# Kernel tuning notes

Measured on AMD Instinct MI355X. Metric: run time of the kernel, lower is better.

## Reference

```python
import jax, jax.numpy as jnp
import numpy as np

N_USERS = 100000
N_MOVIES = 50000
N_EDGES = 1000000
IN_CH, HID, OUT = 64, 128, 64


def setup_inputs() -> dict:
    key = jax.random.key(0)
    ks = jax.random.split(key, 8)
    N = N_USERS + N_MOVIES
    return {
        "edge_index": jax.random.randint(ks[0], (2, N_EDGES), 0, N, dtype=jnp.int64)
        if jax.config.jax_enable_x64 else jax.random.randint(ks[0], (2, N_EDGES), 0, N, dtype=jnp.int32),
        "user_emb": jax.random.normal(ks[1], (N_USERS, IN_CH), jnp.float32) * 0.05,
        "movie_emb": jax.random.normal(ks[2], (N_MOVIES, IN_CH), jnp.float32) * 0.05,
        "W1l": jax.random.normal(ks[3], (HID, IN_CH), jnp.float32) * 0.05,
        "b1": jnp.zeros((HID,), jnp.float32),
        "W1r": jax.random.normal(ks[4], (HID, IN_CH), jnp.float32) * 0.05,
        "W2l": jax.random.normal(ks[5], (OUT, HID), jnp.float32) * 0.05,
        "b2": jnp.zeros((OUT,), jnp.float32),
        "W2r": jax.random.normal(ks[6], (OUT, HID), jnp.float32) * 0.05,
    }


def _sage_conv(x, src, dst, Wl, bl, Wr, num_nodes):
    # mean-aggregate neighbor (source) features at destination nodes
    msg_sum = jax.ops.segment_sum(x[src], dst, num_segments=num_nodes)  # [N, d_in]
    deg = jax.ops.segment_sum(jnp.ones(src.shape, x.dtype), dst, num_segments=num_nodes)
    agg = msg_sum / jnp.maximum(deg, 1.0)[:, None]
    # out = lin_l(agg) + lin_r(x); lin_l carries the bias (PyG SAGEConv default)
    return agg @ Wl.T + bl + x @ Wr.T


def reference(edge_index, user_emb, movie_emb, W1l, b1, W1r, W2l, b2, W2r):
    N = user_emb.shape[0] + movie_emb.shape[0]
    src, dst = edge_index[0], edge_index[1]
    x = jnp.concatenate([user_emb, movie_emb], axis=0)  # [N, in_ch]
    x = jax.nn.relu(_sage_conv(x, src, dst, W1l, b1, W1r, N))  # dropout = identity (eval)
    x = _sage_conv(x, src, dst, W2l, b2, W2r, N)
    return x[:N_USERS], x[N_USERS:]
```

## Files before the change

### kernel.cpp

```cpp
#include <hip/hip_runtime.h>

constexpr int N_USERS  = 100000;
constexpr int N_MOVIES = 50000;
constexpr int N_NODES  = N_USERS + N_MOVIES;
constexpr int N_EDGES  = 1000000;

typedef __attribute__((ext_vector_type(8))) short bf16x8;
typedef __attribute__((ext_vector_type(8))) unsigned short usx8;
typedef __attribute__((ext_vector_type(4))) float f32x4;

__device__ inline unsigned short bf16_rne(float x) {
    unsigned u = __float_as_uint(x);
    unsigned r = (u + 0x7FFF + ((u >> 16) & 1)) >> 16;
    return (unsigned short)r;
}
__device__ inline float bf16_to_f(short v) {
    return __uint_as_float(((unsigned)(unsigned short)v) << 16);
}

__global__ __launch_bounds__(256) void csr_ord(const int* __restrict__ ei,
                                               int* __restrict__ cnt,
                                               int* __restrict__ ord) {
    int t  = blockIdx.x * 256 + threadIdx.x;
    int e0 = t * 4;
    if (e0 + 3 < N_EDGES) {
        int4 d = *(const int4*)&ei[N_EDGES + e0];
        int4 o;
        o.x = atomicAdd(&cnt[d.x], 1);
        o.y = atomicAdd(&cnt[d.y], 1);
        o.z = atomicAdd(&cnt[d.z], 1);
        o.w = atomicAdd(&cnt[d.w], 1);
        *(int4*)&ord[e0] = o;
    } else {
        for (int e = e0; e < N_EDGES; ++e)
            ord[e] = atomicAdd(&cnt[ei[N_EDGES + e]], 1);
    }
}

__global__ __launch_bounds__(256) void csr_scatter(const int* __restrict__ ei,
                                                   const int* __restrict__ row_ptr,
                                                   const int* __restrict__ ord,
                                                   int* __restrict__ srclist) {
    int t  = blockIdx.x * 256 + threadIdx.x;
    int e0 = t * 4;
    if (e0 + 3 < N_EDGES) {
        int4 s = *(const int4*)&ei[e0];
        int4 d = *(const int4*)&ei[N_EDGES + e0];
        int4 o = *(const int4*)&ord[e0];
        srclist[row_ptr[d.x] + o.x] = s.x;
        srclist[row_ptr[d.y] + o.y] = s.y;
        srclist[row_ptr[d.z] + o.z] = s.z;
        srclist[row_ptr[d.w] + o.w] = s.w;
    } else {
        for (int e = e0; e < N_EDGES; ++e)
            srclist[row_ptr[ei[N_EDGES + e]] + ord[e]] = ei[e];
    }
}

__global__ __launch_bounds__(256) void scan1(const int* __restrict__ cnt,
                                             int* __restrict__ part,
                                             int* __restrict__ bsum) {
    __shared__ int sh[256];
    int t = threadIdx.x, b = blockIdx.x;
    int base = b * 1024 + t * 4;
    int v[4]; int s = 0;
#pragma unroll
    for (int j = 0; j < 4; ++j) {
        int i = base + j;
        v[j] = (i < N_NODES) ? cnt[i] : 0;
        s += v[j];
    }
    sh[t] = s; __syncthreads();
    for (int off = 1; off < 256; off <<= 1) {
        int x = (t >= off) ? sh[t - off] : 0;
        __syncthreads();
        sh[t] += x;
        __syncthreads();
    }
    int run = sh[t] - s;
#pragma unroll
    for (int j = 0; j < 4; ++j) {
        int i = base + j;
        if (i < N_NODES) part[i] = run;
        run += v[j];
    }
    if (t == 255) bsum[b] = sh[255];
}

__global__ __launch_bounds__(256) void scan2(int* __restrict__ bsum, int nb) {
    __shared__ int sh[256];
    int t = threadIdx.x;
    int v = (t < nb) ? bsum[t] : 0;
    sh[t] = v; __syncthreads();
    for (int off = 1; off < 256; off <<= 1) {
        int x = (t >= off) ? sh[t - off] : 0;
        __syncthreads();
        sh[t] += x;
        __syncthreads();
    }
    if (t < nb) bsum[t] = sh[t] - v;
}

__global__ __launch_bounds__(256) void scan3(int* __restrict__ row_ptr,
                                             const int* __restrict__ bsum) {
    int t = threadIdx.x, b = blockIdx.x;
    int base = b * 1024 + t * 4;
    int add = bsum[b];
#pragma unroll
    for (int j = 0; j < 4; ++j) {
        int i = base + j;
        if (i < N_NODES) row_ptr[i] += add;
    }
    if (b == 0 && t == 0) row_ptr[N_NODES] = N_EDGES;
}

__global__ __launch_bounds__(256) void prepack_w(const float* __restrict__ W1l,
                                                 const float* __restrict__ W1r,
                                                 const float* __restrict__ W2l,
                                                 const float* __restrict__ W2r,
                                                 unsigned short* __restrict__ wb) {
    int i = blockIdx.x * 256 + threadIdx.x;
    if (i >= 2 * 128 * 128) return;
    int layer = i >> 14;
    int r     = i & 16383;
    int kc    = r >> 12;
    int oc    = (r >> 9) & 7;
    int lane  = (r >> 3) & 63;
    int j     = r & 7;
    int k = kc * 32 + (lane >> 4) * 8 + j;
    int o = oc * 16 + (lane & 15);
    float v;
    if (layer == 0) v = (k < 64) ? W1l[o * 64 + k] : W1r[o * 64 + (k - 64)];
    else            v = (o < 64) ? W2l[o * 128 + k] : W2r[(o - 64) * 128 + k];
    wb[i] = bf16_rne(v);
}

__global__ __launch_bounds__(256) void pack_x(const float* __restrict__ ue,
                                              const float* __restrict__ me,
                                              unsigned short* __restrict__ xb) {
    int i = blockIdx.x * 256 + threadIdx.x;
    if (i >= N_NODES * 8) return;
    int n = i >> 3, c = (i & 7) * 8;
    const float* src = (n < N_USERS) ? &ue[(size_t)n * 64 + c]
                                     : &me[(size_t)(n - N_USERS) * 64 + c];
    float4 v0 = *(const float4*)src;
    float4 v1 = *(const float4*)(src + 4);
    usx8 r;
    r[0] = bf16_rne(v0.x); r[1] = bf16_rne(v0.y);
    r[2] = bf16_rne(v0.z); r[3] = bf16_rne(v0.w);
    r[4] = bf16_rne(v1.x); r[5] = bf16_rne(v1.y);
    r[6] = bf16_rne(v1.z); r[7] = bf16_rne(v1.w);
    *(usx8*)&xb[(size_t)n * 64 + c] = r;
}

__global__ __launch_bounds__(256) void gather1(const int* __restrict__ row_ptr,
                                               const int* __restrict__ srclist,
                                               const unsigned short* __restrict__ xb,
                                               unsigned short* __restrict__ aggb) {
    int gid = blockIdx.x * 256 + threadIdx.x;
    int n = gid >> 3, l = gid & 7;
    if (n >= N_NODES) return;
    int s0 = row_ptr[n], s1 = row_ptr[n + 1];
    float acc[8] = {};
    for (int i = s0; i < s1; ++i) {
        int a = srclist[i];
        bf16x8 v = *(const bf16x8*)&xb[(size_t)a * 64 + l * 8];
#pragma unroll
        for (int j = 0; j < 8; ++j) acc[j] += bf16_to_f(v[j]);
    }
    float inv = 1.0f / fmaxf((float)(s1 - s0), 1.0f);
    usx8 r;
#pragma unroll
    for (int j = 0; j < 8; ++j) r[j] = bf16_rne(acc[j] * inv);
    *(usx8*)&aggb[(size_t)n * 64 + l * 8] = r;
}

__global__ __launch_bounds__(256) void gather2_final(const int* __restrict__ row_ptr,
                                                     const int* __restrict__ srclist,
                                                     const unsigned short* __restrict__ zb,
                                                     const float* __restrict__ wf,
                                                     const float* __restrict__ b2,
                                                     float* __restrict__ out) {
    int gid = blockIdx.x * 256 + threadIdx.x;
    int n = gid >> 3, l = gid & 7;
    if (n >= N_NODES) return;
    int s0 = row_ptr[n], s1 = row_ptr[n + 1];
    float acc[8] = {};
    for (int i = s0; i < s1; ++i) {
        int a = srclist[i];
        bf16x8 v = *(const bf16x8*)&zb[(size_t)a * 64 + l * 8];
#pragma unroll
        for (int j = 0; j < 8; ++j) acc[j] += bf16_to_f(v[j]);
    }
    float inv = 1.0f / fmaxf((float)(s1 - s0), 1.0f);
    float4 w0 = *(const float4*)&wf[(size_t)n * 64 + l * 8];
    float4 w1 = *(const float4*)&wf[(size_t)n * 64 + l * 8 + 4];
    float4 c0 = *(const float4*)&b2[l * 8];
    float4 c1 = *(const float4*)&b2[l * 8 + 4];
    float4 r0, r1;
    r0.x = acc[0] * inv + w0.x + c0.x;
    r0.y = acc[1] * inv + w0.y + c0.y;
    r0.z = acc[2] * inv + w0.z + c0.z;
    r0.w = acc[3] * inv + w0.w + c0.w;
    r1.x = acc[4] * inv + w1.x + c1.x;
    r1.y = acc[5] * inv + w1.y + c1.y;
    r1.z = acc[6] * inv + w1.z + c1.z;
    r1.w = acc[7] * inv + w1.w + c1.w;
    *(float4*)&out[(size_t)n * 64 + l * 8]     = r0;
    *(float4*)&out[(size_t)n * 64 + l * 8 + 4] = r1;
}

template <bool LAYER1>
__global__ __launch_bounds__(256) void gemm_bf16(const unsigned short* Ab,
                                                 const unsigned short* __restrict__ xb,
                                                 const unsigned short* __restrict__ wb,
                                                 const float* __restrict__ bias,
                                                 unsigned short* outb,
                                                 float* outf) {
    const int tid  = threadIdx.x;
    const int w    = tid >> 6;
    const int lane = tid & 63;
    const int n0   = blockIdx.x * 128 + w * 32;
    const int lr   = lane & 15;
    const int lg   = lane >> 4;

    f32x4 acc[2][8] = {};
    const int wbase = LAYER1 ? 0 : 2048;

    for (int kc = 0; kc < 4; ++kc) {
        const int k0 = kc * 32 + lg * 8;
        bf16x8 a[2];
#pragma unroll
        for (int f = 0; f < 2; ++f) {
            int node = n0 + f * 16 + lr;
            bf16x8 z = {};
            a[f] = z;
            if (node < N_NODES) {
                const unsigned short* ap;
                if (LAYER1)
                    ap = (k0 < 64) ? &Ab[(size_t)node * 64 + k0]
                                   : &xb[(size_t)node * 64 + (k0 - 64)];
                else
                    ap = &Ab[(size_t)node * 128 + k0];
                a[f] = *(const bf16x8*)ap;
            }
        }
#pragma unroll
        for (int oc = 0; oc < 8; ++oc) {
            size_t widx = ((size_t)(wbase + (kc * 8 + oc) * 64 + lane)) * 8;
            bf16x8 wfrag = *(const bf16x8*)&wb[widx];
#pragma unroll
            for (int f = 0; f < 2; ++f)
                acc[f][oc] = __builtin_amdgcn_mfma_f32_16x16x32_bf16(a[f], wfrag, acc[f][oc], 0, 0, 0);
        }
    }

#pragma unroll
    for (int f = 0; f < 2; ++f) {
#pragma unroll
        for (int oc = 0; oc < 8; ++oc) {
            int col = oc * 16 + lr;
            float b = LAYER1 ? bias[col] : 0.f;
#pragma unroll
            for (int i = 0; i < 4; ++i) {
                int row = n0 + f * 16 + lg * 4 + i;
                if (row < N_NODES) {
                    float v = acc[f][oc][i] + b;
                    if (LAYER1) {
                        outb[(size_t)row * 128 + col] = bf16_rne(fmaxf(v, 0.f));
                    } else {
                        if (oc < 4) outb[(size_t)row * 64 + col] = bf16_rne(v);
                        else        outf[(size_t)row * 64 + (col - 64)] = v;
                    }
                }
            }
        }
    }
}

extern "C" void kernel_launch(void* const* d_in, const int* in_sizes, int n_in,
                              void* d_out, int out_size, void* d_ws, size_t ws_size,
                              hipStream_t stream) {
    const int*   ei  = (const int*)d_in[0];
    const float* ue  = (const float*)d_in[1];
    const float* me  = (const float*)d_in[2];
    const float* W1l = (const float*)d_in[3];
    const float* b1  = (const float*)d_in[4];
    const float* W1r = (const float*)d_in[5];
    const float* W2l = (const float*)d_in[6];
    const float* b2  = (const float*)d_in[7];
    const float* W2r = (const float*)d_in[8];
    float* out = (float*)d_out;

    char* p = (char*)d_ws;
    int* row_ptr = (int*)p;                   p += (((N_NODES + 1) * 4) + 255) / 256 * 256;
    int* srclist = (int*)p;                   p += (size_t)N_EDGES * 4;
    int* ord     = (int*)p;                   p += (size_t)N_EDGES * 4;
    unsigned short* wb = (unsigned short*)p;  p += 2 * 128 * 128 * 2;
    unsigned short* xb = (unsigned short*)p;  p += (size_t)N_NODES * 64 * 2;
    unsigned short* h1b = (unsigned short*)p; p += (size_t)N_NODES * 128 * 2;
    unsigned short* zb  = (unsigned short*)p; p += (size_t)N_NODES * 64 * 2;
    float* wf = (float*)h1b;
    int* cnt  = (int*)h1b;
    int* bsum = cnt + N_NODES;
    unsigned short* aggb = (unsigned short*)out;

    const int NB  = (N_NODES + 1023) / 1024;
    const int EB4 = (N_EDGES / 4 + 255) / 256;

    hipMemsetAsync(cnt, 0, N_NODES * sizeof(int), stream);
    csr_ord<<<EB4, 256, 0, stream>>>(ei, cnt, ord);
    scan1<<<NB, 256, 0, stream>>>(cnt, row_ptr, bsum);
    scan2<<<1, 256, 0, stream>>>(bsum, NB);
    scan3<<<NB, 256, 0, stream>>>(row_ptr, bsum);
    csr_scatter<<<EB4, 256, 0, stream>>>(ei, row_ptr, ord, srclist);
    prepack_w<<<(2 * 128 * 128 + 255) / 256, 256, 0, stream>>>(W1l, W1r, W2l, W2r, wb);
    pack_x<<<(N_NODES * 8 + 255) / 256, 256, 0, stream>>>(ue, me, xb);

    int gblocks = (N_NODES * 8 + 255) / 256;
    int mblocks = (N_NODES + 127) / 128;

    gather1<<<gblocks, 256, 0, stream>>>(row_ptr, srclist, xb, aggb);
    gemm_bf16<true><<<mblocks, 256, 0, stream>>>(aggb, xb, wb, b1, h1b, nullptr);
    gemm_bf16<false><<<mblocks, 256, 0, stream>>>(h1b, nullptr, wb, nullptr, zb, wf);
    gather2_final<<<gblocks, 256, 0, stream>>>(row_ptr, srclist, zb, wf, b2, out);
}
```

Measured before the change: 206.8 us.

## Fuse both GEMM layers via LDS and merge prep and scan kernels

The two layer GEMMs now run in one kernel: the ReLU'd hidden tile is kept in shared memory and fed straight into the second GEMM, so the 128-wide hidden activation never goes to global memory. Edge counting, weight prepacking and embedding conversion are merged into one launch, and the second and third scan passes are combined, with each block redoing the small block-sum scan itself. The root-term output of layer 2 is now stored as bf16 instead of fp32, which halves that traffic but adds rounding error to the final output. Fewer launches and less global memory traffic are the aim, at the cost of more LDS per block, which may lower occupancy.

```diff
diff --git a/kernel.cpp b/kernel.cpp
--- a/kernel.cpp
+++ b/kernel.cpp
@@ -18,23 +18,127 @@
     return __uint_as_float(((unsigned)(unsigned short)v) << 16);
 }
 
-__global__ __launch_bounds__(256) void csr_ord(const int* __restrict__ ei,
-                                               int* __restrict__ cnt,
-                                               int* __restrict__ ord) {
-    int t  = blockIdx.x * 256 + threadIdx.x;
-    int e0 = t * 4;
-    if (e0 + 3 < N_EDGES) {
-        int4 d = *(const int4*)&ei[N_EDGES + e0];
-        int4 o;
-        o.x = atomicAdd(&cnt[d.x], 1);
-        o.y = atomicAdd(&cnt[d.y], 1);
-        o.z = atomicAdd(&cnt[d.z], 1);
-        o.w = atomicAdd(&cnt[d.w], 1);
-        *(int4*)&ord[e0] = o;
-    } else {
-        for (int e = e0; e < N_EDGES; ++e)
-            ord[e] = atomicAdd(&cnt[ei[N_EDGES + e]], 1);
-    }
+constexpr int ORD_BLKS = (N_EDGES / 8 + 255) / 256;
+constexpr int PW_BLKS  = (2 * 128 * 128) / 256;
+constexpr int PX_BLKS  = (N_NODES * 8 + 255) / 256;
+
+__global__ __launch_bounds__(256) void prep_fused(const int* __restrict__ ei,
+                                                  int* __restrict__ cnt,
+                                                  int* __restrict__ ord,
+                                                  const float* __restrict__ W1l,
+                                                  const float* __restrict__ W1r,
+                                                  const float* __restrict__ W2l,
+                                                  const float* __restrict__ W2r,
+                                                  unsigned short* __restrict__ wb,
+                                                  const float* __restrict__ ue,
+                                                  const float* __restrict__ me,
+                                                  unsigned short* __restrict__ xb) {
+    const int ob = blockIdx.x;
+    if (ob < ORD_BLKS) {
+        int t  = ob * 256 + threadIdx.x;
+        int e0 = t * 8;
+        if (e0 + 7 < N_EDGES) {
+            int4 d0 = *(const int4*)&ei[N_EDGES + e0];
+            int4 d1 = *(const int4*)&ei[N_EDGES + e0 + 4];
+            int4 o0, o1;
+            o0.x = atomicAdd(&cnt[d0.x], 1);
+            o0.y = atomicAdd(&cnt[d0.y], 1);
+            o0.z = atomicAdd(&cnt[d0.z], 1);
+            o0.w = atomicAdd(&cnt[d0.w], 1);
+            o1.x = atomicAdd(&cnt[d1.x], 1);
+            o1.y = atomicAdd(&cnt[d1.y], 1);
+            o1.z = atomicAdd(&cnt[d1.z], 1);
+            o1.w = atomicAdd(&cnt[d1.w], 1);
+            *(int4*)&ord[e0]     = o0;
+            *(int4*)&ord[e0 + 4] = o1;
+        } else {
+            for (int e = e0; e < N_EDGES; ++e)
+                ord[e] = atomicAdd(&cnt[ei[N_EDGES + e]], 1);
+        }
+        return;
+    }
+    if (ob < ORD_BLKS + PW_BLKS) {
+        int i = (ob - ORD_BLKS) * 256 + threadIdx.x;
+        int layer = i >> 14;
+        int r     = i & 16383;
+        int kc    = r >> 12;
+        int oc    = (r >> 9) & 7;
+        int lane  = (r >> 3) & 63;
+        int j     = r & 7;
+        int k = kc * 32 + (lane >> 4) * 8 + j;
+        int o = oc * 16 + (lane & 15);
+        float v;
+        if (layer == 0) v = (k < 64) ? W1l[o * 64 + k] : W1r[o * 64 + (k - 64)];
+        else            v = (o < 64) ? W2l[o * 128 + k] : W2r[(o - 64) * 128 + k];
+        wb[i] = bf16_rne(v);
+        return;
+    }
+    int i = (ob - ORD_BLKS - PW_BLKS) * 256 + threadIdx.x;
+    if (i >= N_NODES * 8) return;
+    int n = i >> 3, c = (i & 7) * 8;
+    const float* src = (n < N_USERS) ? &ue[(size_t)n * 64 + c]
+                                     : &me[(size_t)(n - N_USERS) * 64 + c];
+    float4 v0 = *(const float4*)src;
+    float4 v1 = *(const float4*)(src + 4);
+    usx8 r;
+    r[0] = bf16_rne(v0.x); r[1] = bf16_rne(v0.y);
+    r[2] = bf16_rne(v0.z); r[3] = bf16_rne(v0.w);
+    r[4] = bf16_rne(v1.x); r[5] = bf16_rne(v1.y);
+    r[6] = bf16_rne(v1.z); r[7] = bf16_rne(v1.w);
+    *(usx8*)&xb[(size_t)n * 64 + c] = r;
+}
+
+__global__ __launch_bounds__(256) void scan1(const int* __restrict__ cnt,
+                                             int* __restrict__ part,
+                                             int* __restrict__ bsum) {
+    __shared__ int sh[256];
+    int t = threadIdx.x, b = blockIdx.x;
+    int base = b * 1024 + t * 4;
+    int v[4]; int s = 0;
+#pragma unroll
+    for (int j = 0; j < 4; ++j) {
+        int i = base + j;
+        v[j] = (i < N_NODES) ? cnt[i] : 0;
+        s += v[j];
+    }
+    sh[t] = s; __syncthreads();
+    for (int off = 1; off < 256; off <<= 1) {
+        int x = (t >= off) ? sh[t - off] : 0;
+        __syncthreads();
+        sh[t] += x;
+        __syncthreads();
+    }
+    int run = sh[t] - s;
+#pragma unroll
+    for (int j = 0; j < 4; ++j) {
+        int i = base + j;
+        if (i < N_NODES) part[i] = run;
+        run += v[j];
+    }
+    if (t == 255) bsum[b] = sh[255];
+}
+
+__global__ __launch_bounds__(256) void scan23(int* __restrict__ row_ptr,
+                                              const int* __restrict__ bsum,
+                                              int nb) {
+    __shared__ int sh[256];
+    int t = threadIdx.x, b = blockIdx.x;
+    int v = (t < nb) ? bsum[t] : 0;
+    sh[t] = v; __syncthreads();
+    for (int off = 1; off < 256; off <<= 1) {
+        int x = (t >= off) ? sh[t - off] : 0;
+        __syncthreads();
+        sh[t] += x;
+        __syncthreads();
+    }
+    int add = (b == 0) ? 0 : sh[b - 1];
+    int base = b * 1024 + t * 4;
+#pragma unroll
+    for (int j = 0; j < 4; ++j) {
+        int i = base + j;
+        if (i < N_NODES) row_ptr[i] += add;
+    }
+    if (b == 0 && t == 0) row_ptr[N_NODES] = N_EDGES;
 }
 
 __global__ __launch_bounds__(256) void csr_scatter(const int* __restrict__ ei,
@@ -57,102 +161,6 @@
     }
 }
 
-__global__ __launch_bounds__(256) void scan1(const int* __restrict__ cnt,
-                                             int* __restrict__ part,
-                                             int* __restrict__ bsum) {
-    __shared__ int sh[256];
-    int t = threadIdx.x, b = blockIdx.x;
-    int base = b * 1024 + t * 4;
-    int v[4]; int s = 0;
-#pragma unroll
-    for (int j = 0; j < 4; ++j) {
-        int i = base + j;
-        v[j] = (i < N_NODES) ? cnt[i] : 0;
-        s += v[j];
-    }
-    sh[t] = s; __syncthreads();
-    for (int off = 1; off < 256; off <<= 1) {
-        int x = (t >= off) ? sh[t - off] : 0;
-        __syncthreads();
-        sh[t] += x;
-        __syncthreads();
-    }
-    int run = sh[t] - s;
-#pragma unroll
-    for (int j = 0; j < 4; ++j) {
-        int i = base + j;
-        if (i < N_NODES) part[i] = run;
-        run += v[j];
-    }
-    if (t == 255) bsum[b] = sh[255];
-}
-
-__global__ __launch_bounds__(256) void scan2(int* __restrict__ bsum, int nb) {
-    __shared__ int sh[256];
-    int t = threadIdx.x;
-    int v = (t < nb) ? bsum[t] : 0;
-    sh[t] = v; __syncthreads();
-    for (int off = 1; off < 256; off <<= 1) {
-        int x = (t >= off) ? sh[t - off] : 0;
-        __syncthreads();
-        sh[t] += x;
-        __syncthreads();
-    }
-    if (t < nb) bsum[t] = sh[t] - v;
-}
-
-__global__ __launch_bounds__(256) void scan3(int* __restrict__ row_ptr,
-                                             const int* __restrict__ bsum) {
-    int t = threadIdx.x, b = blockIdx.x;
-    int base = b * 1024 + t * 4;
-    int add = bsum[b];
-#pragma unroll
-    for (int j = 0; j < 4; ++j) {
-        int i = base + j;
-        if (i < N_NODES) row_ptr[i] += add;
-    }
-    if (b == 0 && t == 0) row_ptr[N_NODES] = N_EDGES;
-}
-
-__global__ __launch_bounds__(256) void prepack_w(const float* __restrict__ W1l,
-                                                 const float* __restrict__ W1r,
-                                                 const float* __restrict__ W2l,
-                                                 const float* __restrict__ W2r,
-                                                 unsigned short* __restrict__ wb) {
-    int i = blockIdx.x * 256 + threadIdx.x;
-    if (i >= 2 * 128 * 128) return;
-    int layer = i >> 14;
-    int r     = i & 16383;
-    int kc    = r >> 12;
-    int oc    = (r >> 9) & 7;
-    int lane  = (r >> 3) & 63;
-    int j     = r & 7;
-    int k = kc * 32 + (lane >> 4) * 8 + j;
-    int o = oc * 16 + (lane & 15);
-    float v;
-    if (layer == 0) v = (k < 64) ? W1l[o * 64 + k] : W1r[o * 64 + (k - 64)];
-    else            v = (o < 64) ? W2l[o * 128 + k] : W2r[(o - 64) * 128 + k];
-    wb[i] = bf16_rne(v);
-}
-
-__global__ __launch_bounds__(256) void pack_x(const float* __restrict__ ue,
-                                              const float* __restrict__ me,
-                                              unsigned short* __restrict__ xb) {
-    int i = blockIdx.x * 256 + threadIdx.x;
-    if (i >= N_NODES * 8) return;
-    int n = i >> 3, c = (i & 7) * 8;
-    const float* src = (n < N_USERS) ? &ue[(size_t)n * 64 + c]
-                                     : &me[(size_t)(n - N_USERS) * 64 + c];
-    float4 v0 = *(const float4*)src;
-    float4 v1 = *(const float4*)(src + 4);
-    usx8 r;
-    r[0] = bf16_rne(v0.x); r[1] = bf16_rne(v0.y);
-    r[2] = bf16_rne(v0.z); r[3] = bf16_rne(v0.w);
-    r[4] = bf16_rne(v1.x); r[5] = bf16_rne(v1.y);
-    r[6] = bf16_rne(v1.z); r[7] = bf16_rne(v1.w);
-    *(usx8*)&xb[(size_t)n * 64 + c] = r;
-}
-
 __global__ __launch_bounds__(256) void gather1(const int* __restrict__ row_ptr,
                                                const int* __restrict__ srclist,
                                                const unsigned short* __restrict__ xb,
@@ -178,7 +186,7 @@
 __global__ __launch_bounds__(256) void gather2_final(const int* __restrict__ row_ptr,
                                                      const int* __restrict__ srclist,
                                                      const unsigned short* __restrict__ zb,
-                                                     const float* __restrict__ wf,
+                                                     const unsigned short* __restrict__ wfb,
                                                      const float* __restrict__ b2,
                                                      float* __restrict__ out) {
     int gid = blockIdx.x * 256 + threadIdx.x;
@@ -193,84 +201,110 @@
         for (int j = 0; j < 8; ++j) acc[j] += bf16_to_f(v[j]);
     }
     float inv = 1.0f / fmaxf((float)(s1 - s0), 1.0f);
-    float4 w0 = *(const float4*)&wf[(size_t)n * 64 + l * 8];
-    float4 w1 = *(const float4*)&wf[(size_t)n * 64 + l * 8 + 4];
+    bf16x8 wv = *(const bf16x8*)&wfb[(size_t)n * 64 + l * 8];
     float4 c0 = *(const float4*)&b2[l * 8];
     float4 c1 = *(const float4*)&b2[l * 8 + 4];
     float4 r0, r1;
-    r0.x = acc[0] * inv + w0.x + c0.x;
-    r0.y = acc[1] * inv + w0.y + c0.y;
-    r0.z = acc[2] * inv + w0.z + c0.z;
-    r0.w = acc[3] * inv + w0.w + c0.w;
-    r1.x = acc[4] * inv + w1.x + c1.x;
-    r1.y = acc[5] * inv + w1.y + c1.y;
-    r1.z = acc[6] * inv + w1.z + c1.z;
-    r1.w = acc[7] * inv + w1.w + c1.w;
+    r0.x = acc[0] * inv + bf16_to_f(wv[0]) + c0.x;
+    r0.y = acc[1] * inv + bf16_to_f(wv[1]) + c0.y;
+    r0.z = acc[2] * inv + bf16_to_f(wv[2]) + c0.z;
+    r0.w = acc[3] * inv + bf16_to_f(wv[3]) + c0.w;
+    r1.x = acc[4] * inv + bf16_to_f(wv[4]) + c1.x;
+    r1.y = acc[5] * inv + bf16_to_f(wv[5]) + c1.y;
+    r1.z = acc[6] * inv + bf16_to_f(wv[6]) + c1.z;
+    r1.w = acc[7] * inv + bf16_to_f(wv[7]) + c1.w;
     *(float4*)&out[(size_t)n * 64 + l * 8]     = r0;
     *(float4*)&out[(size_t)n * 64 + l * 8 + 4] = r1;
 }
 
-template <bool LAYER1>
-__global__ __launch_bounds__(256) void gemm_bf16(const unsigned short* Ab,
-                                                 const unsigned short* __restrict__ xb,
-                                                 const unsigned short* __restrict__ wb,
-                                                 const float* __restrict__ bias,
-                                                 unsigned short* outb,
-                                                 float* outf) {
+__global__ __launch_bounds__(256) void gemm_fused(const unsigned short* __restrict__ aggb,
+                                                  const unsigned short* __restrict__ xb,
+                                                  const unsigned short* __restrict__ wb,
+                                                  const float* __restrict__ b1,
+                                                  unsigned short* __restrict__ zb,
+                                                  unsigned short* __restrict__ wfb) {
+    __shared__ unsigned short hs[128][136];
     const int tid  = threadIdx.x;
     const int w    = tid >> 6;
     const int lane = tid & 63;
-    const int n0   = blockIdx.x * 128 + w * 32;
+    const int n0   = blockIdx.x * 128;
+    const int nw   = n0 + w * 32;
     const int lr   = lane & 15;
     const int lg   = lane >> 4;
 
-    f32x4 acc[2][8] = {};
-    const int wbase = LAYER1 ? 0 : 2048;
-
-    for (int kc = 0; kc < 4; ++kc) {
-        const int k0 = kc * 32 + lg * 8;
-        bf16x8 a[2];
+    {
+        f32x4 acc[2][8] = {};
+        for (int kc = 0; kc < 4; ++kc) {
+            const int k0 = kc * 32 + lg * 8;
+            bf16x8 a[2];
+#pragma unroll
+            for (int f = 0; f < 2; ++f) {
+                int node = nw + f * 16 + lr;
+                bf16x8 z = {};
+                a[f] = z;
+                if (node < N_NODES) {
+                    const unsigned short* ap = (k0 < 64)
+                        ? &aggb[(size_t)node * 64 + k0]
+                        : &xb[(size_t)node * 64 + (k0 - 64)];
+                    a[f] = *(const bf16x8*)ap;
+                }
+            }
+#pragma unroll
+            for (int oc = 0; oc < 8; ++oc) {
+                size_t widx = ((size_t)((kc * 8 + oc) * 64 + lane)) * 8;
+                bf16x8 wfrag = *(const bf16x8*)&wb[widx];
+#pragma unroll
+                for (int f = 0; f < 2; ++f)
+                    acc[f][oc] = __builtin_amdgcn_mfma_f32_16x16x32_bf16(a[f], wfrag, acc[f][oc], 0, 0, 0);
+            }
+        }
 #pragma unroll
         for (int f = 0; f < 2; ++f) {
-            int node = n0 + f * 16 + lr;
-            bf16x8 z = {};
-            a[f] = z;
-            if (node < N_NODES) {
-                const unsigned short* ap;
-                if (LAYER1)
-                    ap = (k0 < 64) ? &Ab[(size_t)node * 64 + k0]
-                                   : &xb[(size_t)node * 64 + (k0 - 64)];
-                else
-                    ap = &Ab[(size_t)node * 128 + k0];
-                a[f] = *(const bf16x8*)ap;
-            }
-        }
-#pragma unroll
-        for (int oc = 0; oc < 8; ++oc) {
-            size_t widx = ((size_t)(wbase + (kc * 8 + oc) * 64 + lane)) * 8;
-            bf16x8 wfrag = *(const bf16x8*)&wb[widx];
-#pragma unroll
-            for (int f = 0; f < 2; ++f)
-                acc[f][oc] = __builtin_amdgcn_mfma_f32_16x16x32_bf16(a[f], wfrag, acc[f][oc], 0, 0, 0);
-        }
-    }
-
-#pragma unroll
-    for (int f = 0; f < 2; ++f) {
-#pragma unroll
-        for (int oc = 0; oc < 8; ++oc) {
-            int col = oc * 16 + lr;
-            float b = LAYER1 ? bias[col] : 0.f;
-#pragma unroll
-            for (int i = 0; i < 4; ++i) {
-                int row = n0 + f * 16 + lg * 4 + i;
-                if (row < N_NODES) {
-                    float v = acc[f][oc][i] + b;
-                    if (LAYER1) {
-                        outb[(size_t)row * 128 + col] = bf16_rne(fmaxf(v, 0.f));
-                    } else {
-                        if (oc < 4) outb[(size_t)row * 64 + col] = bf16_rne(v);
-                        else        outf[(size_t)row * 64 + (col - 64)] = v;
+#pragma unroll
+            for (int oc = 0; oc < 8; ++oc) {
+                int col = oc * 16 + lr;
+                float b = b1[col];
+#pragma unroll
+                for (int i = 0; i < 4; ++i) {
+                    int rowl = w * 32 + f * 16 + lg * 4 + i;
+                    hs[rowl][col] = bf16_rne(fmaxf(acc[f][oc][i] + b, 0.f));
+                }
+            }
+        }
+    }
+    __syncthreads();
+
+    {
+        f32x4 acc[2][8] = {};
+        for (int kc = 0; kc < 4; ++kc) {
+            const int k0 = kc * 32 + lg * 8;
+            bf16x8 a[2];
+#pragma unroll
+            for (int f = 0; f < 2; ++f) {
+                int rowl = w * 32 + f * 16 + lr;
+                a[f] = *(const bf16x8*)&hs[rowl][k0];
+            }
+#pragma unroll
+            for (int oc = 0; oc < 8; ++oc) {
+                size_t widx = ((size_t)(2048 + (kc * 8 + oc) * 64 + lane)) * 8;
+                bf16x8 wfrag = *(const bf16x8*)&wb[widx];
+#pragma unroll
+                for (int f = 0; f < 2; ++f)
+                    acc[f][oc] = __builtin_amdgcn_mfma_f32_16x16x32_bf16(a[f], wfrag, acc[f][oc], 0, 0, 0);
+            }
+        }
+#pragma unroll
+        for (int f = 0; f < 2; ++f) {
+#pragma unroll
+            for (int oc = 0; oc < 8; ++oc) {
+                int col = oc * 16 + lr;
+#pragma unroll
+                for (int i = 0; i < 4; ++i) {
+                    int row = nw + f * 16 + lg * 4 + i;
+                    if (row < N_NODES) {
+                        unsigned short v = bf16_rne(acc[f][oc][i]);
+                        if (oc < 4) zb[(size_t)row * 64 + col] = v;
+                        else        wfb[(size_t)row * 64 + (col - 64)] = v;
                     }
                 }
             }
@@ -296,32 +330,27 @@
     int* row_ptr = (int*)p;                   p += (((N_NODES + 1) * 4) + 255) / 256 * 256;
     int* srclist = (int*)p;                   p += (size_t)N_EDGES * 4;
     int* ord     = (int*)p;                   p += (size_t)N_EDGES * 4;
-    unsigned short* wb = (unsigned short*)p;  p += 2 * 128 * 128 * 2;
-    unsigned short* xb = (unsigned short*)p;  p += (size_t)N_NODES * 64 * 2;
-    unsigned short* h1b = (unsigned short*)p; p += (size_t)N_NODES * 128 * 2;
+    unsigned short* wb  = (unsigned short*)p; p += 2 * 128 * 128 * 2;
+    unsigned short* xb  = (unsigned short*)p; p += (size_t)N_NODES * 64 * 2;
     unsigned short* zb  = (unsigned short*)p; p += (size_t)N_NODES * 64 * 2;
-    float* wf = (float*)h1b;
-    int* cnt  = (int*)h1b;
+    unsigned short* wfb = (unsigned short*)p; p += (size_t)N_NODES * 64 * 2;
+    int* cnt  = (int*)zb;
     int* bsum = cnt + N_NODES;
     unsigned short* aggb = (unsigned short*)out;
 
-    const int NB  = (N_NODES + 1023) / 1024;
-    const int EB4 = (N_EDGES / 4 + 255) / 256;
+    const int NB = (N_NODES + 1023) / 1024;
 
     hipMemsetAsync(cnt, 0, N_NODES * sizeof(int), stream);
-    csr_ord<<<EB4, 256, 0, stream>>>(ei, cnt, ord);
+    prep_fused<<<ORD_BLKS + PW_BLKS + PX_BLKS, 256, 0, stream>>>(
+        ei, cnt, ord, W1l, W1r, W2l, W2r, wb, ue, me, xb);
     scan1<<<NB, 256, 0, stream>>>(cnt, row_ptr, bsum);
-    scan2<<<1, 256, 0, stream>>>(bsum, NB);
-    scan3<<<NB, 256, 0, stream>>>(row_ptr, bsum);
-    csr_scatter<<<EB4, 256, 0, stream>>>(ei, row_ptr, ord, srclist);
-    prepack_w<<<(2 * 128 * 128 + 255) / 256, 256, 0, stream>>>(W1l, W1r, W2l, W2r, wb);
-    pack_x<<<(N_NODES * 8 + 255) / 256, 256, 0, stream>>>(ue, me, xb);
+    scan23<<<NB, 256, 0, stream>>>(row_ptr, bsum, NB);
+    csr_scatter<<<(N_EDGES / 4 + 255) / 256, 256, 0, stream>>>(ei, row_ptr, ord, srclist);
 
     int gblocks = (N_NODES * 8 + 255) / 256;
     int mblocks = (N_NODES + 127) / 128;
 
     gather1<<<gblocks, 256, 0, stream>>>(row_ptr, srclist, xb, aggb);
-    gemm_bf16<true><<<mblocks, 256, 0, stream>>>(aggb, xb, wb, b1, h1b, nullptr);
-    gemm_bf16<false><<<mblocks, 256, 0, stream>>>(h1b, nullptr, wb, nullptr, zb, wf);
-    gather2_final<<<gblocks, 256, 0, stream>>>(row_ptr, srclist, zb, wf, b2, out);
-}
+    gemm_fused<<<mblocks, 256, 0, stream>>>(aggb, xb, wb, b1, zb, wfb);
+    gather2_final<<<gblocks, 256, 0, stream>>>(row_ptr, srclist, zb, wfb, b2, out);
+}
```

After: 177.2 us. 1.17x faster.
